# Kernel optimization log

Measured on AMD Instinct MI355X. Metric: run time of the kernel, lower is better.

Reference implementation:

```python
import jax, jax.numpy as jnp
import numpy as np

NUM_KERNELS = 8
KERNEL_SIZES = [2 ** i for i in range(1, NUM_KERNELS + 1)]


def setup_inputs() -> dict:
    key = jax.random.key(0)
    x = jax.random.uniform(key, (32, 1, 1024, 1024), dtype=jnp.float32)
    return {"x": x}


def _plogp(p):
    # p * log2(p), safely 0 at p == 0 (log2(1) == 0)
    ps = jnp.where(p > 0, p, 1.0)
    return ps * jnp.log2(ps)


def reference(x):
    # Slice_windows(num_kernels=8, mode='entropy', to_binary=False)
    B, C, H, W = x.shape
    cols = []
    for k in KERNEL_SIZES:
        if k > H or k > W:
            cols.append(jnp.zeros((B,), dtype=x.dtype))
            continue
        Hk, Wk = H // k, W // k
        n = k * k * C
        # non-overlapping window sums == sum-pooling with stride k
        xs = x[:, :, : Hk * k, : Wk * k].reshape(B, C, Hk, k, Wk, k)
        s = xs.sum(axis=(1, 3, 5))            # (B, Hk, Wk)
        p1 = s / n
        p0 = 1.0 - p1
        entropy = -_plogp(p0) - _plogp(p1)    # Shannon entropy per window
        cols.append(entropy.mean(axis=(1, 2)))  # average over all windows
    return jnp.stack(cols, axis=1)  # (B, num_kernels)
```

## Files before the change

### kernel.cpp

```cpp
#include <hip/hip_runtime.h>

#define IMG 1024

__device__ __forceinline__ float ent(float s, float inv_n) {
    float p1 = s * inv_n;
    float p0 = 1.0f - p1;
    float l1 = (p1 > 0.0f) ? __log2f(p1) : 0.0f;
    float l0 = (p0 > 0.0f) ? __log2f(p0) : 0.0f;
    return -(p0 * l0 + p1 * l1);
}

__device__ __forceinline__ float bfly_sum(float v) {
#pragma unroll
    for (int m = 32; m >= 1; m >>= 1) v += __shfl_xor(v, m);
    return v;
}

__global__ __launch_bounds__(256, 4) void slice_k1(const float* __restrict__ x,
                                                   float* __restrict__ ws) {
    const int b    = blockIdx.x >> 6;
    const int tile = blockIdx.x & 63;
    const int tr = tile >> 3, tc = tile & 7;
    const int t = threadIdx.x;
    const int w = t >> 6, lane = t & 63;
    const int wr = w >> 1, wc = w & 1;
    const int cy = lane >> 3, cx = lane & 7;

    const int row0 = tr * 128 + wr * 64 + cy * 8;
    const int col0 = tc * 128 + wc * 64 + cx * 8;
    const float* p = x + (size_t)b * (IMG * IMG) + (size_t)row0 * IMG + col0;

    float4 va[8], vb[8];
#pragma unroll
    for (int i = 0; i < 8; ++i) {
        va[i] = *(const float4*)(p + (size_t)i * IMG);
        vb[i] = *(const float4*)(p + (size_t)i * IMG + 4);
    }

    float e2sum = 0.f, e4sum = 0.f;
    float s4[2][2] = {{0.f, 0.f}, {0.f, 0.f}};
#pragma unroll
    for (int ry = 0; ry < 4; ++ry) {
        float4 a0 = va[2 * ry], a1 = va[2 * ry + 1];
        float4 b0 = vb[2 * ry], b1 = vb[2 * ry + 1];
        float sA = a0.x + a0.y + a1.x + a1.y;
        float sB = a0.z + a0.w + a1.z + a1.w;
        float sC = b0.x + b0.y + b1.x + b1.y;
        float sD = b0.z + b0.w + b1.z + b1.w;
        e2sum += ent(sA, 0.25f) + ent(sB, 0.25f) + ent(sC, 0.25f) + ent(sD, 0.25f);
        s4[ry >> 1][0] += sA + sB;
        s4[ry >> 1][1] += sC + sD;
    }
    float s8 = 0.f;
#pragma unroll
    for (int i = 0; i < 2; ++i)
#pragma unroll
        for (int j = 0; j < 2; ++j) { e4sum += ent(s4[i][j], 1.f / 16.f); s8 += s4[i][j]; }
    float e8 = ent(s8, 1.f / 64.f);

    float s16 = s8 + __shfl_xor(s8, 1);  s16 += __shfl_xor(s16, 8);
    float e16 = ent(s16, 1.f / 256.f);
    float s32 = s16 + __shfl_xor(s16, 2); s32 += __shfl_xor(s32, 16);
    float e32 = ent(s32, 1.f / 1024.f);
    float s64 = s32 + __shfl_xor(s32, 4); s64 += __shfl_xor(s64, 32);
    float e64 = ent(s64, 1.f / 4096.f);

    float E2 = bfly_sum(e2sum);
    float E4 = bfly_sum(e4sum);
    float E8 = bfly_sum(e8);
    float E16 = e16 + __shfl_xor(e16, 2); E16 += __shfl_xor(E16, 4);
    E16 += __shfl_xor(E16, 16);   E16 += __shfl_xor(E16, 32);
    float E32 = e32 + __shfl_xor(e32, 4); E32 += __shfl_xor(E32, 32);

    __shared__ float wl[4][8];
    if (lane == 0) {
        wl[w][0] = E2;  wl[w][1] = E4;  wl[w][2] = E8;
        wl[w][3] = E16; wl[w][4] = E32; wl[w][5] = e64; wl[w][6] = s64;
    }
    __syncthreads();
    if (t < 8) {
        float r;
        if (t < 6) {
            r = wl[0][t] + wl[1][t] + wl[2][t] + wl[3][t];
        } else {
            float s128 = wl[0][6] + wl[1][6] + wl[2][6] + wl[3][6];
            r = (t == 6) ? ent(s128, 1.f / 16384.f) : s128;
        }
        ws[(size_t)blockIdx.x * 8 + t] = r;
    }
}

__global__ __launch_bounds__(64) void slice_k2(const float* __restrict__ ws,
                                               float* __restrict__ out) {
    const int b = blockIdx.x, l = threadIdx.x;
    const float4* g = (const float4*)(ws + ((size_t)b * 64 + l) * 8);
    float4 u0 = g[0], u1 = g[1];
    float v[8] = {u0.x, u0.y, u0.z, u0.w, u1.x, u1.y, u1.z, u1.w};

    float s256 = v[7] + __shfl_xor(v[7], 1); s256 += __shfl_xor(s256, 8);
    float e256 = ent(s256, 1.f / 65536.f);
    float E256 = e256 + __shfl_xor(e256, 2); E256 += __shfl_xor(E256, 4);
    E256 += __shfl_xor(E256, 16);  E256 += __shfl_xor(E256, 32);

    float sums[7];
#pragma unroll
    for (int j = 0; j < 7; ++j) sums[j] = bfly_sum(v[j]);

    if (l == 0) {
        const float invw[7] = {1.f / 262144.f, 1.f / 65536.f, 1.f / 16384.f,
                               1.f / 4096.f,   1.f / 1024.f,  1.f / 256.f, 1.f / 64.f};
        float* o = out + b * 8;
#pragma unroll
        for (int j = 0; j < 7; ++j) o[j] = sums[j] * invw[j];
        o[7] = E256 * (1.f / 16.f);
    }
}

extern "C" void kernel_launch(void* const* d_in, const int* in_sizes, int n_in,
                              void* d_out, int out_size, void* d_ws, size_t ws_size,
                              hipStream_t stream) {
    const float* x = (const float*)d_in[0];
    float* out = (float*)d_out;
    float* ws  = (float*)d_ws;

    slice_k1<<<32 * 64, 256, 0, stream>>>(x, ws);
    slice_k2<<<32, 64, 0, stream>>>(ws, out);
}
```

Before: 185.1 us.

## Remap lanes to row-interleaved float4 columns with nontemporal loads and shuffle reductions

Changes the thread-to-data mapping so each lane loads one 16-byte column chunk from 16 rows spaced 4 apart. Each wave instruction now covers contiguous 256-byte row segments, which improves coalescing. Window sums are combined across lanes with many more cross-lane shuffles, and duplicated entropy contributions are scaled down afterwards. Loads use nontemporal hints to avoid polluting the cache. In exchange the kernel does far more shuffles and redundant entropy evaluations per lane, which raises ALU and log work.

```diff
diff --git a/kernel.cpp b/kernel.cpp
--- a/kernel.cpp
+++ b/kernel.cpp
@@ -1,6 +1,8 @@
 #include <hip/hip_runtime.h>
 
 #define IMG 1024
+
+typedef float v4f __attribute__((ext_vector_type(4)));
 
 __device__ __forceinline__ float ent(float s, float inv_n) {
     float p1 = s * inv_n;
@@ -24,53 +26,73 @@
     const int t = threadIdx.x;
     const int w = t >> 6, lane = t & 63;
     const int wr = w >> 1, wc = w & 1;
-    const int cy = lane >> 3, cx = lane & 7;
+    const int c0 = lane >> 4;
+    const int c4 = lane & 15;
 
-    const int row0 = tr * 128 + wr * 64 + cy * 8;
-    const int col0 = tc * 128 + wc * 64 + cx * 8;
+    const int row0 = tr * 128 + wr * 64 + c0;
+    const int col0 = tc * 128 + wc * 64 + c4 * 4;
     const float* p = x + (size_t)b * (IMG * IMG) + (size_t)row0 * IMG + col0;
 
-    float4 va[8], vb[8];
+    v4f v[16];
 #pragma unroll
-    for (int i = 0; i < 8; ++i) {
-        va[i] = *(const float4*)(p + (size_t)i * IMG);
-        vb[i] = *(const float4*)(p + (size_t)i * IMG + 4);
+    for (int i = 0; i < 16; ++i)
+        v[i] = __builtin_nontemporal_load((const v4f*)(p + (size_t)(4 * i) * IMG));
+
+    float e2 = 0.f, e4 = 0.f;
+    float s4[16];
+#pragma unroll
+    for (int i = 0; i < 16; ++i) {
+        float sx = v[i].x + v[i].y;
+        float sz = v[i].z + v[i].w;
+        float w2x = sx + __shfl_xor(sx, 16);
+        float w2z = sz + __shfl_xor(sz, 16);
+        e2 += ent(w2x, 0.25f) + ent(w2z, 0.25f);
+        float cs = sx + sz;
+        float r4 = cs + __shfl_xor(cs, 16);
+        float w4 = r4 + __shfl_xor(r4, 32);
+        e4 += ent(w4, 1.f / 16.f);
+        s4[i] = w4;
     }
 
-    float e2sum = 0.f, e4sum = 0.f;
-    float s4[2][2] = {{0.f, 0.f}, {0.f, 0.f}};
+    float e8 = 0.f;
+    float s8[8];
 #pragma unroll
-    for (int ry = 0; ry < 4; ++ry) {
-        float4 a0 = va[2 * ry], a1 = va[2 * ry + 1];
-        float4 b0 = vb[2 * ry], b1 = vb[2 * ry + 1];
-        float sA = a0.x + a0.y + a1.x + a1.y;
-        float sB = a0.z + a0.w + a1.z + a1.w;
-        float sC = b0.x + b0.y + b1.x + b1.y;
-        float sD = b0.z + b0.w + b1.z + b1.w;
-        e2sum += ent(sA, 0.25f) + ent(sB, 0.25f) + ent(sC, 0.25f) + ent(sD, 0.25f);
-        s4[ry >> 1][0] += sA + sB;
-        s4[ry >> 1][1] += sC + sD;
+    for (int j = 0; j < 8; ++j) {
+        float u = s4[2 * j] + s4[2 * j + 1];
+        float s = u + __shfl_xor(u, 1);
+        e8 += ent(s, 1.f / 64.f);
+        s8[j] = s;
     }
-    float s8 = 0.f;
+
+    float e16 = 0.f;
+    float s16[4];
 #pragma unroll
-    for (int i = 0; i < 2; ++i)
+    for (int q = 0; q < 4; ++q) {
+        float u = s8[2 * q] + s8[2 * q + 1];
+        float s = u + __shfl_xor(u, 2);
+        e16 += ent(s, 1.f / 256.f);
+        s16[q] = s;
+    }
+
+    float e32 = 0.f;
+    float s32[2];
 #pragma unroll
-        for (int j = 0; j < 2; ++j) { e4sum += ent(s4[i][j], 1.f / 16.f); s8 += s4[i][j]; }
-    float e8 = ent(s8, 1.f / 64.f);
+    for (int h = 0; h < 2; ++h) {
+        float u = s16[2 * h] + s16[2 * h + 1];
+        float s = u + __shfl_xor(u, 4);
+        e32 += ent(s, 1.f / 1024.f);
+        s32[h] = s;
+    }
 
-    float s16 = s8 + __shfl_xor(s8, 1);  s16 += __shfl_xor(s16, 8);
-    float e16 = ent(s16, 1.f / 256.f);
-    float s32 = s16 + __shfl_xor(s16, 2); s32 += __shfl_xor(s32, 16);
-    float e32 = ent(s32, 1.f / 1024.f);
-    float s64 = s32 + __shfl_xor(s32, 4); s64 += __shfl_xor(s64, 32);
+    float u64 = s32[0] + s32[1];
+    float s64 = u64 + __shfl_xor(u64, 8);
     float e64 = ent(s64, 1.f / 4096.f);
 
-    float E2 = bfly_sum(e2sum);
-    float E4 = bfly_sum(e4sum);
-    float E8 = bfly_sum(e8);
-    float E16 = e16 + __shfl_xor(e16, 2); E16 += __shfl_xor(E16, 4);
-    E16 += __shfl_xor(E16, 16);   E16 += __shfl_xor(E16, 32);
-    float E32 = e32 + __shfl_xor(e32, 4); E32 += __shfl_xor(E32, 32);
+    float E2  = bfly_sum(e2)  * 0.5f;
+    float E4  = bfly_sum(e4)  * 0.25f;
+    float E8  = bfly_sum(e8)  * 0.125f;
+    float E16 = bfly_sum(e16) * (1.f / 16.f);
+    float E32 = bfly_sum(e32) * (1.f / 32.f);
 
     __shared__ float wl[4][8];
     if (lane == 0) {
```

New measurement: 181.1 us. 2.2% less time.
